# Kernel tuning notes

Hardware: AMD Instinct MI355X
Metric: run time of the kernel (lower is better)

## Reference

```python
import jax, jax.numpy as jnp
import numpy as np

B, C, H, W = 128, 3, 256, 256


def setup_inputs() -> dict:
    key = jax.random.key(0)
    k1, k2, k3, k4 = jax.random.split(key, 4)
    img = jax.random.uniform(k1, (B, C, H, W), jnp.float32)
    # init in the module: rot=PI, trans=0, scale=1, shear=0; add small noise
    rot = jnp.pi + 0.5 * jax.random.normal(k2, (B, 1), jnp.float32)
    trans = 0.1 * jax.random.normal(k3, (B, 2), jnp.float32)
    scale = jnp.ones((B, 1), jnp.float32)
    shear = 0.1 * jax.random.normal(k4, (B, 2), jnp.float32)
    return {"img": img, "rot": rot, "trans": trans, "scale": scale, "shear": shear}


def _theta(rot, trans, scale, shear):
    # 2x3 affine matrix per sample: A = scale * R(rot) @ Shear, last col = trans
    r = rot[:, 0]
    s = scale[:, 0]
    c, sn = jnp.cos(r), jnp.sin(r)
    shx, shy = shear[:, 0], shear[:, 1]
    a00 = s * (c - sn * shy)
    a01 = s * (c * shx - sn)
    a10 = s * (sn + c * shy)
    a11 = s * (sn * shx + c)
    row0 = jnp.stack([a00, a01, trans[:, 0]], axis=-1)  # [B,3]
    row1 = jnp.stack([a10, a11, trans[:, 1]], axis=-1)  # [B,3]
    return jnp.stack([row0, row1], axis=1)  # [B,2,3]


def _affine_grid(theta, Hc, Wc):
    # normalized coords, align_corners=False convention
    ys = (2.0 * (jnp.arange(Hc, dtype=jnp.float32) + 0.5) / Hc) - 1.0
    xs = (2.0 * (jnp.arange(Wc, dtype=jnp.float32) + 0.5) / Wc) - 1.0
    gx, gy = jnp.meshgrid(xs, ys)  # [H,W]
    base = jnp.stack([gx, gy, jnp.ones_like(gx)], axis=-1)  # [H,W,3]
    return jnp.einsum('bij,hwj->bhwi', theta, base)  # [B,H,W,2] -> (x,y)


def _grid_sample(img, grid):
    # bilinear, zeros padding, align_corners=False
    Bc, Cc, Hc, Wc = img.shape
    ix = ((grid[..., 0] + 1.0) * Wc - 1.0) / 2.0
    iy = ((grid[..., 1] + 1.0) * Hc - 1.0) / 2.0
    x0 = jnp.floor(ix); y0 = jnp.floor(iy)
    x1 = x0 + 1.0; y1 = y0 + 1.0
    wx1 = ix - x0; wx0 = 1.0 - wx1
    wy1 = iy - y0; wy0 = 1.0 - wy1
    flat = img.reshape(Bc, Cc, Hc * Wc)

    def gather(xi, yi, w):
        valid = (xi >= 0) & (xi <= Wc - 1) & (yi >= 0) & (yi <= Hc - 1)
        xc = jnp.clip(xi, 0, Wc - 1).astype(jnp.int32)
        yc = jnp.clip(yi, 0, Hc - 1).astype(jnp.int32)
        idx = (yc * Wc + xc).reshape(Bc, 1, -1)  # [B,1,H*W]
        vals = jnp.take_along_axis(flat, idx, axis=2)  # [B,C,H*W]
        wm = (w * valid.astype(w.dtype)).reshape(Bc, 1, -1)
        return vals * wm

    out = (gather(x0, y0, wx0 * wy0) + gather(x1, y0, wx1 * wy0)
           + gather(x0, y1, wx0 * wy1) + gather(x1, y1, wx1 * wy1))
    return out.reshape(Bc, Cc, Hc, Wc)


def reference(img, rot, trans, scale, shear):
    theta = _theta(rot, trans, scale, shear)
    grid = _affine_grid(theta, img.shape[2], img.shape[3])
    return _grid_sample(img, grid)
```

## Files before the change

kernel.cpp:

```cpp
#include <hip/hip_runtime.h>
#include <math.h>

#define BATCH 128
#define CHAN  3
#define IMH   256
#define IMW   256
#define NXCD  8
#define TW    32
#define TH    16

#define BH_T   42
#define NC_MAX 44
#define ROWSTR 132

__global__ __launch_bounds__(256) void affine_sample_kernel(
        const float* __restrict__ img,
        const float* __restrict__ rot,
        const float* __restrict__ trans,
        const float* __restrict__ scale,
        const float* __restrict__ shear,
        float* __restrict__ out) {
    __shared__ float tile[BH_T * ROWSTR];

    const int NBLK = BATCH * 64;
    const int p = blockIdx.x;
    const int L = (p & (NXCD - 1)) * (NBLK / NXCD) + (p >> 3);

    const int b  = L >> 6;
    const int tl = L & 63;
    const int w0 = (tl & 7) * TW;
    const int h0 = (tl >> 3) * (2 * TH);

    const float r   = rot[b];
    const float s   = scale[b];
    const float shx = shear[2 * b + 0];
    const float shy = shear[2 * b + 1];
    const float txr = trans[2 * b + 0];
    const float tyr = trans[2 * b + 1];
    const float c  = __cosf(r);
    const float sn = __sinf(r);
    const float a00 = s * (c - sn * shy);
    const float a01 = s * (c * shx - sn);
    const float a10 = s * (sn + c * shy);
    const float a11 = s * (sn * shx + c);
    const float g0x = 1.0f / (float)IMW - 1.0f;
    const float g0y = 1.0f / (float)IMH - 1.0f;
    const float Cx = ((a00 * g0x + a01 * g0y + txr + 1.0f) * (float)IMW - 1.0f) * 0.5f;
    const float Cy = ((a10 * g0x + a11 * g0y + tyr + 1.0f) * (float)IMH - 1.0f) * 0.5f;
    const float hx = 15.5f * fabsf(a00) + 7.5f * fabsf(a01);
    const float hy = 15.5f * fabsf(a10) + 7.5f * fabsf(a11);

    const int t  = threadIdx.x;
    const int wq = w0 + (t & 31);
    const int hoff = (t >> 5) << 1;
    const int lx2 = (t & 31) << 1;
    const int lyr = t >> 5;
    const int plane = IMH * IMW;
    const float* ibase = img + (size_t)(b * CHAN) * plane;

    for (int half = 0; half < 2; ++half) {
        const int h0h = h0 + half * TH;

        const float ixc = Cx + a00 * ((float)w0 + 15.5f) + a01 * ((float)h0h + 7.5f);
        const float iyc = Cy + a10 * ((float)w0 + 15.5f) + a11 * ((float)h0h + 7.5f);
        const int xlu = (int)floorf(ixc - hx);
        const int xhu = (int)floorf(ixc + hx) + 1;
        const int ylu = (int)floorf(iyc - hy);
        const int yhu = (int)floorf(iyc + hy) + 1;
        const bool interior = (xlu >= 1) & (xhu <= IMW - 2) &
                              (ylu >= 1) & (yhu <= IMH - 2);

        const int x_lo = min(max(xlu, 0), IMW - 1);
        const int x_hi = min(max(xhu, 0), IMW - 1);
        const int y_lo = min(max(ylu, 0), IMH - 1);
        const int y_hi = min(max(yhu, 0), IMH - 1);
        const int xs  = (x_lo - 1) & ~1;
        const int ys  = y_lo - 1;
        const int ncs = x_hi + 2 - xs;
        const int nrs = y_hi + 2 - ys;
        const bool fits = (ncs <= NC_MAX) & (nrs <= BH_T);

        const int hq = h0h + hoff;
        const float ixa = Cx + a00 * (float)wq + a01 * (float)hq;
        const float iya = Cy + a10 * (float)wq + a11 * (float)hq;
        const float ixb = ixa + a01;
        const float iyb = iya + a11;

        const float x0fa = floorf(ixa), y0fa = floorf(iya);
        const float x0fb = floorf(ixb), y0fb = floorf(iyb);
        const float wx1a = ixa - x0fa, wy1a = iya - y0fa;
        const float wx1b = ixb - x0fb, wy1b = iyb - y0fb;
        const float wx0a = 1.0f - wx1a, wy0a = 1.0f - wy1a;
        const float wx0b = 1.0f - wx1b, wy0b = 1.0f - wy1b;

        float w00a, w10a, w01a, w11a, w00b, w10b, w01b, w11b;
        if (interior) {
            w00a = wx0a * wy0a; w10a = wx1a * wy0a;
            w01a = wx0a * wy1a; w11a = wx1a * wy1a;
            w00b = wx0b * wy0b; w10b = wx1b * wy0b;
            w01b = wx0b * wy1b; w11b = wx1b * wy1b;
        } else {
            const bool vx0a = (x0fa >= 0.0f) & (x0fa <= (float)(IMW - 1));
            const bool vx1a = (x0fa >= -1.0f) & (x0fa <= (float)(IMW - 2));
            const bool vy0a = (y0fa >= 0.0f) & (y0fa <= (float)(IMH - 1));
            const bool vy1a = (y0fa >= -1.0f) & (y0fa <= (float)(IMH - 2));
            w00a = (vx0a && vy0a) ? (wx0a * wy0a) : 0.0f;
            w10a = (vx1a && vy0a) ? (wx1a * wy0a) : 0.0f;
            w01a = (vx0a && vy1a) ? (wx0a * wy1a) : 0.0f;
            w11a = (vx1a && vy1a) ? (wx1a * wy1a) : 0.0f;
            const bool vx0b = (x0fb >= 0.0f) & (x0fb <= (float)(IMW - 1));
            const bool vx1b = (x0fb >= -1.0f) & (x0fb <= (float)(IMW - 2));
            const bool vy0b = (y0fb >= 0.0f) & (y0fb <= (float)(IMH - 1));
            const bool vy1b = (y0fb >= -1.0f) & (y0fb <= (float)(IMH - 2));
            w00b = (vx0b && vy0b) ? (wx0b * wy0b) : 0.0f;
            w10b = (vx1b && vy0b) ? (wx1b * wy0b) : 0.0f;
            w01b = (vx0b && vy1b) ? (wx0b * wy1b) : 0.0f;
            w11b = (vx1b && vy1b) ? (wx1b * wy1b) : 0.0f;
        }

        const int x0ia = (int)x0fa, y0ia = (int)y0fa;
        const int x0ib = (int)x0fb, y0ib = (int)y0fb;
        const int obase = (b * CHAN) * plane + hq * IMW + wq;

        if (half) __syncthreads();

        if (fits) {
            const int nrd = (nrs + 7) >> 3;
            const bool wcol = lx2 < ncs;
            const int xg = min(max(xs + lx2, 0), IMW - 2);
            for (int rr = 0; rr < nrd; ++rr) {
                const int dy = (rr << 3) + lyr;
                if (wcol & (dy < nrs)) {
                    const int yg = min(max(ys + dy, 0), IMH - 1);
                    const float* src = ibase + yg * IMW + xg;
                    const float2 v0 = *(const float2*)(src);
                    const float2 v1 = *(const float2*)(src + plane);
                    const float2 v2 = *(const float2*)(src + 2 * plane);
                    float* dst = &tile[dy * ROWSTR + lx2 * 3];
                    dst[0] = v0.x; dst[1] = v1.x; dst[2] = v2.x;
                    dst[3] = v0.y; dst[4] = v1.y; dst[5] = v2.y;
                }
            }
        }
        __syncthreads();

        if (fits) {
            int rxa, rya, rxb, ryb;
            if (interior) {
                rxa = x0ia - xs;  rya = y0ia - ys;
                rxb = x0ib - xs;  ryb = y0ib - ys;
            } else {
                rxa = min(max(x0ia - xs, 0), ncs - 2);
                rya = min(max(y0ia - ys, 0), nrs - 2);
                rxb = min(max(x0ib - xs, 0), ncs - 2);
                ryb = min(max(y0ib - ys, 0), nrs - 2);
            }
            const float* tpa = &tile[rya * ROWSTR + rxa * 3];
            const float* tpb = &tile[ryb * ROWSTR + rxb * 3];
#pragma unroll
            for (int cc = 0; cc < CHAN; ++cc) {
                const float va = w00a * tpa[cc]          + w10a * tpa[cc + 3]
                               + w01a * tpa[cc + ROWSTR] + w11a * tpa[cc + ROWSTR + 3];
                const float vb = w00b * tpb[cc]          + w10b * tpb[cc + 3]
                               + w01b * tpb[cc + ROWSTR] + w11b * tpb[cc + ROWSTR + 3];
                out[obase + cc * plane]       = va;
                out[obase + cc * plane + IMW] = vb;
            }
        } else {
            const int x0ca = min(max(x0ia, 0), IMW - 1);
            const int x1ca = min(max(x0ia + 1, 0), IMW - 1);
            const int y0ca = min(max(y0ia, 0), IMH - 1);
            const int y1ca = min(max(y0ia + 1, 0), IMH - 1);
            const int x0cb = min(max(x0ib, 0), IMW - 1);
            const int x1cb = min(max(x0ib + 1, 0), IMW - 1);
            const int y0cb = min(max(y0ib, 0), IMH - 1);
            const int y1cb = min(max(y0ib + 1, 0), IMH - 1);
#pragma unroll
            for (int cc = 0; cc < CHAN; ++cc) {
                const float* p2 = ibase + cc * plane;
                const float va = w00a * p2[y0ca * IMW + x0ca] + w10a * p2[y0ca * IMW + x1ca]
                               + w01a * p2[y1ca * IMW + x0ca] + w11a * p2[y1ca * IMW + x1ca];
                const float vb = w00b * p2[y0cb * IMW + x0cb] + w10b * p2[y0cb * IMW + x1cb]
                               + w01b * p2[y1cb * IMW + x0cb] + w11b * p2[y1cb * IMW + x1cb];
                out[obase + cc * plane]       = va;
                out[obase + cc * plane + IMW] = vb;
            }
        }
    }
}

extern "C" void kernel_launch(void* const* d_in, const int* in_sizes, int n_in,
                              void* d_out, int out_size, void* d_ws, size_t ws_size,
                              hipStream_t stream) {
    const float* img   = (const float*)d_in[0];
    const float* rot   = (const float*)d_in[1];
    const float* trans = (const float*)d_in[2];
    const float* scale = (const float*)d_in[3];
    const float* shear = (const float*)d_in[4];
    float* out = (float*)d_out;

    const int nblocks = BATCH * 64;
    affine_sample_kernel<<<nblocks, 256, 0, stream>>>(img, rot, trans, scale,
                                                      shear, out);
}
```

Measured before the change: 43.37 us.

## Split blocks to one tile each and software-pipeline the global-to-LDS staging loads

Each block used to process two 32x16 output tiles one after the other. It now handles a single tile, which doubles the grid to 16384 blocks and removes the per-half loop and one barrier. The tile staging loop also prefetches the next row group's float2 loads into registers before it writes the current group to shared memory, so global load latency overlaps with LDS stores. The cost is more blocks, each repeating the per-sample setup math, plus extra registers for the prefetched values.

```diff
diff --git a/kernel.cpp b/kernel.cpp
--- a/kernel.cpp
+++ b/kernel.cpp
@@ -22,14 +22,14 @@
         float* __restrict__ out) {
     __shared__ float tile[BH_T * ROWSTR];
 
-    const int NBLK = BATCH * 64;
+    const int NBLK = BATCH * (IMH / TH) * (IMW / TW);
     const int p = blockIdx.x;
     const int L = (p & (NXCD - 1)) * (NBLK / NXCD) + (p >> 3);
 
-    const int b  = L >> 6;
-    const int tl = L & 63;
+    const int b  = L >> 7;
+    const int tl = L & 127;
     const int w0 = (tl & 7) * TW;
-    const int h0 = (tl >> 3) * (2 * TH);
+    const int h0 = (tl >> 3) * TH;
 
     const float r   = rot[b];
     const float s   = scale[b];
@@ -50,141 +50,145 @@
     const float hx = 15.5f * fabsf(a00) + 7.5f * fabsf(a01);
     const float hy = 15.5f * fabsf(a10) + 7.5f * fabsf(a11);
 
+    const float ixc = Cx + a00 * ((float)w0 + 15.5f) + a01 * ((float)h0 + 7.5f);
+    const float iyc = Cy + a10 * ((float)w0 + 15.5f) + a11 * ((float)h0 + 7.5f);
+    const int xlu = (int)floorf(ixc - hx);
+    const int xhu = (int)floorf(ixc + hx) + 1;
+    const int ylu = (int)floorf(iyc - hy);
+    const int yhu = (int)floorf(iyc + hy) + 1;
+    const bool interior = (xlu >= 1) & (xhu <= IMW - 2) & (ylu >= 1) & (yhu <= IMH - 2);
+
+    const int x_lo = min(max(xlu, 0), IMW - 1);
+    const int x_hi = min(max(xhu, 0), IMW - 1);
+    const int y_lo = min(max(ylu, 0), IMH - 1);
+    const int y_hi = min(max(yhu, 0), IMH - 1);
+    const int xs  = (x_lo - 1) & ~1;
+    const int ys  = y_lo - 1;
+    const int ncs = x_hi + 2 - xs;
+    const int nrs = y_hi + 2 - ys;
+
     const int t  = threadIdx.x;
     const int wq = w0 + (t & 31);
-    const int hoff = (t >> 5) << 1;
-    const int lx2 = (t & 31) << 1;
-    const int lyr = t >> 5;
+    const int hq = h0 + ((t >> 5) << 1);
+    const float ixa = Cx + a00 * (float)wq + a01 * (float)hq;
+    const float iya = Cy + a10 * (float)wq + a11 * (float)hq;
+    const float ixb = ixa + a01;
+    const float iyb = iya + a11;
+
+    const float x0fa = floorf(ixa), y0fa = floorf(iya);
+    const float x0fb = floorf(ixb), y0fb = floorf(iyb);
+    const float wx1a = ixa - x0fa, wy1a = iya - y0fa;
+    const float wx1b = ixb - x0fb, wy1b = iyb - y0fb;
+    const float wx0a = 1.0f - wx1a, wy0a = 1.0f - wy1a;
+    const float wx0b = 1.0f - wx1b, wy0b = 1.0f - wy1b;
+
+    float w00a, w10a, w01a, w11a, w00b, w10b, w01b, w11b;
+    if (interior) {
+        w00a = wx0a * wy0a; w10a = wx1a * wy0a;
+        w01a = wx0a * wy1a; w11a = wx1a * wy1a;
+        w00b = wx0b * wy0b; w10b = wx1b * wy0b;
+        w01b = wx0b * wy1b; w11b = wx1b * wy1b;
+    } else {
+        const bool vx0a = (x0fa >= 0.0f) & (x0fa <= (float)(IMW - 1));
+        const bool vx1a = (x0fa >= -1.0f) & (x0fa <= (float)(IMW - 2));
+        const bool vy0a = (y0fa >= 0.0f) & (y0fa <= (float)(IMH - 1));
+        const bool vy1a = (y0fa >= -1.0f) & (y0fa <= (float)(IMH - 2));
+        w00a = (vx0a && vy0a) ? (wx0a * wy0a) : 0.0f;
+        w10a = (vx1a && vy0a) ? (wx1a * wy0a) : 0.0f;
+        w01a = (vx0a && vy1a) ? (wx0a * wy1a) : 0.0f;
+        w11a = (vx1a && vy1a) ? (wx1a * wy1a) : 0.0f;
+        const bool vx0b = (x0fb >= 0.0f) & (x0fb <= (float)(IMW - 1));
+        const bool vx1b = (x0fb >= -1.0f) & (x0fb <= (float)(IMW - 2));
+        const bool vy0b = (y0fb >= 0.0f) & (y0fb <= (float)(IMH - 1));
+        const bool vy1b = (y0fb >= -1.0f) & (y0fb <= (float)(IMH - 2));
+        w00b = (vx0b && vy0b) ? (wx0b * wy0b) : 0.0f;
+        w10b = (vx1b && vy0b) ? (wx1b * wy0b) : 0.0f;
+        w01b = (vx0b && vy1b) ? (wx0b * wy1b) : 0.0f;
+        w11b = (vx1b && vy1b) ? (wx1b * wy1b) : 0.0f;
+    }
+
+    const int x0ia = (int)x0fa, y0ia = (int)y0fa;
+    const int x0ib = (int)x0fb, y0ib = (int)y0fb;
+
     const int plane = IMH * IMW;
+    const int obase = (b * CHAN) * plane + hq * IMW + wq;
     const float* ibase = img + (size_t)(b * CHAN) * plane;
 
-    for (int half = 0; half < 2; ++half) {
-        const int h0h = h0 + half * TH;
-
-        const float ixc = Cx + a00 * ((float)w0 + 15.5f) + a01 * ((float)h0h + 7.5f);
-        const float iyc = Cy + a10 * ((float)w0 + 15.5f) + a11 * ((float)h0h + 7.5f);
-        const int xlu = (int)floorf(ixc - hx);
-        const int xhu = (int)floorf(ixc + hx) + 1;
-        const int ylu = (int)floorf(iyc - hy);
-        const int yhu = (int)floorf(iyc + hy) + 1;
-        const bool interior = (xlu >= 1) & (xhu <= IMW - 2) &
-                              (ylu >= 1) & (yhu <= IMH - 2);
-
-        const int x_lo = min(max(xlu, 0), IMW - 1);
-        const int x_hi = min(max(xhu, 0), IMW - 1);
-        const int y_lo = min(max(ylu, 0), IMH - 1);
-        const int y_hi = min(max(yhu, 0), IMH - 1);
-        const int xs  = (x_lo - 1) & ~1;
-        const int ys  = y_lo - 1;
-        const int ncs = x_hi + 2 - xs;
-        const int nrs = y_hi + 2 - ys;
-        const bool fits = (ncs <= NC_MAX) & (nrs <= BH_T);
-
-        const int hq = h0h + hoff;
-        const float ixa = Cx + a00 * (float)wq + a01 * (float)hq;
-        const float iya = Cy + a10 * (float)wq + a11 * (float)hq;
-        const float ixb = ixa + a01;
-        const float iyb = iya + a11;
-
-        const float x0fa = floorf(ixa), y0fa = floorf(iya);
-        const float x0fb = floorf(ixb), y0fb = floorf(iyb);
-        const float wx1a = ixa - x0fa, wy1a = iya - y0fa;
-        const float wx1b = ixb - x0fb, wy1b = iyb - y0fb;
-        const float wx0a = 1.0f - wx1a, wy0a = 1.0f - wy1a;
-        const float wx0b = 1.0f - wx1b, wy0b = 1.0f - wy1b;
-
-        float w00a, w10a, w01a, w11a, w00b, w10b, w01b, w11b;
+    if (ncs <= NC_MAX && nrs <= BH_T) {
+        const int lx2 = (t & 31) << 1;
+        const int lyr = t >> 5;
+        const int nrd = (nrs + 7) >> 3;
+        const bool wcol = lx2 < ncs;
+        const int xg = min(max(xs + lx2, 0), IMW - 2);
+
+        float2 v0, v1, v2;
+        {
+            const int dy = lyr;
+            const int yg = min(max(ys + dy, 0), IMH - 1);
+            const float* src = ibase + yg * IMW + xg;
+            if (wcol) { v0 = *(const float2*)(src);
+                        v1 = *(const float2*)(src + plane);
+                        v2 = *(const float2*)(src + 2 * plane); }
+        }
+        for (int rr = 0; rr < nrd; ++rr) {
+            const int dy = (rr << 3) + lyr;
+            float2 n0, n1, n2;
+            const int dyn = dy + 8;
+            if ((rr + 1 < nrd) & wcol & (dyn < nrs)) {
+                const int yg = min(max(ys + dyn, 0), IMH - 1);
+                const float* src = ibase + yg * IMW + xg;
+                n0 = *(const float2*)(src);
+                n1 = *(const float2*)(src + plane);
+                n2 = *(const float2*)(src + 2 * plane);
+            }
+            if (wcol & (dy < nrs)) {
+                float* dst = &tile[dy * ROWSTR + lx2 * 3];
+                dst[0] = v0.x; dst[1] = v1.x; dst[2] = v2.x;
+                dst[3] = v0.y; dst[4] = v1.y; dst[5] = v2.y;
+            }
+            v0 = n0; v1 = n1; v2 = n2;
+        }
+        __syncthreads();
+
+        int rxa, rya, rxb, ryb;
         if (interior) {
-            w00a = wx0a * wy0a; w10a = wx1a * wy0a;
-            w01a = wx0a * wy1a; w11a = wx1a * wy1a;
-            w00b = wx0b * wy0b; w10b = wx1b * wy0b;
-            w01b = wx0b * wy1b; w11b = wx1b * wy1b;
+            rxa = x0ia - xs;  rya = y0ia - ys;
+            rxb = x0ib - xs;  ryb = y0ib - ys;
         } else {
-            const bool vx0a = (x0fa >= 0.0f) & (x0fa <= (float)(IMW - 1));
-            const bool vx1a = (x0fa >= -1.0f) & (x0fa <= (float)(IMW - 2));
-            const bool vy0a = (y0fa >= 0.0f) & (y0fa <= (float)(IMH - 1));
-            const bool vy1a = (y0fa >= -1.0f) & (y0fa <= (float)(IMH - 2));
-            w00a = (vx0a && vy0a) ? (wx0a * wy0a) : 0.0f;
-            w10a = (vx1a && vy0a) ? (wx1a * wy0a) : 0.0f;
-            w01a = (vx0a && vy1a) ? (wx0a * wy1a) : 0.0f;
-            w11a = (vx1a && vy1a) ? (wx1a * wy1a) : 0.0f;
-            const bool vx0b = (x0fb >= 0.0f) & (x0fb <= (float)(IMW - 1));
-            const bool vx1b = (x0fb >= -1.0f) & (x0fb <= (float)(IMW - 2));
-            const bool vy0b = (y0fb >= 0.0f) & (y0fb <= (float)(IMH - 1));
-            const bool vy1b = (y0fb >= -1.0f) & (y0fb <= (float)(IMH - 2));
-            w00b = (vx0b && vy0b) ? (wx0b * wy0b) : 0.0f;
-            w10b = (vx1b && vy0b) ? (wx1b * wy0b) : 0.0f;
-            w01b = (vx0b && vy1b) ? (wx0b * wy1b) : 0.0f;
-            w11b = (vx1b && vy1b) ? (wx1b * wy1b) : 0.0f;
-        }
-
-        const int x0ia = (int)x0fa, y0ia = (int)y0fa;
-        const int x0ib = (int)x0fb, y0ib = (int)y0fb;
-        const int obase = (b * CHAN) * plane + hq * IMW + wq;
-
-        if (half) __syncthreads();
-
-        if (fits) {
-            const int nrd = (nrs + 7) >> 3;
-            const bool wcol = lx2 < ncs;
-            const int xg = min(max(xs + lx2, 0), IMW - 2);
-            for (int rr = 0; rr < nrd; ++rr) {
-                const int dy = (rr << 3) + lyr;
-                if (wcol & (dy < nrs)) {
-                    const int yg = min(max(ys + dy, 0), IMH - 1);
-                    const float* src = ibase + yg * IMW + xg;
-                    const float2 v0 = *(const float2*)(src);
-                    const float2 v1 = *(const float2*)(src + plane);
-                    const float2 v2 = *(const float2*)(src + 2 * plane);
-                    float* dst = &tile[dy * ROWSTR + lx2 * 3];
-                    dst[0] = v0.x; dst[1] = v1.x; dst[2] = v2.x;
-                    dst[3] = v0.y; dst[4] = v1.y; dst[5] = v2.y;
-                }
-            }
-        }
-        __syncthreads();
-
-        if (fits) {
-            int rxa, rya, rxb, ryb;
-            if (interior) {
-                rxa = x0ia - xs;  rya = y0ia - ys;
-                rxb = x0ib - xs;  ryb = y0ib - ys;
-            } else {
-                rxa = min(max(x0ia - xs, 0), ncs - 2);
-                rya = min(max(y0ia - ys, 0), nrs - 2);
-                rxb = min(max(x0ib - xs, 0), ncs - 2);
-                ryb = min(max(y0ib - ys, 0), nrs - 2);
-            }
-            const float* tpa = &tile[rya * ROWSTR + rxa * 3];
-            const float* tpb = &tile[ryb * ROWSTR + rxb * 3];
+            rxa = min(max(x0ia - xs, 0), ncs - 2);
+            rya = min(max(y0ia - ys, 0), nrs - 2);
+            rxb = min(max(x0ib - xs, 0), ncs - 2);
+            ryb = min(max(y0ib - ys, 0), nrs - 2);
+        }
+        const float* tpa = &tile[rya * ROWSTR + rxa * 3];
+        const float* tpb = &tile[ryb * ROWSTR + rxb * 3];
 #pragma unroll
-            for (int cc = 0; cc < CHAN; ++cc) {
-                const float va = w00a * tpa[cc]          + w10a * tpa[cc + 3]
-                               + w01a * tpa[cc + ROWSTR] + w11a * tpa[cc + ROWSTR + 3];
-                const float vb = w00b * tpb[cc]          + w10b * tpb[cc + 3]
-                               + w01b * tpb[cc + ROWSTR] + w11b * tpb[cc + ROWSTR + 3];
-                out[obase + cc * plane]       = va;
-                out[obase + cc * plane + IMW] = vb;
-            }
-        } else {
-            const int x0ca = min(max(x0ia, 0), IMW - 1);
-            const int x1ca = min(max(x0ia + 1, 0), IMW - 1);
-            const int y0ca = min(max(y0ia, 0), IMH - 1);
-            const int y1ca = min(max(y0ia + 1, 0), IMH - 1);
-            const int x0cb = min(max(x0ib, 0), IMW - 1);
-            const int x1cb = min(max(x0ib + 1, 0), IMW - 1);
-            const int y0cb = min(max(y0ib, 0), IMH - 1);
-            const int y1cb = min(max(y0ib + 1, 0), IMH - 1);
+        for (int cc = 0; cc < CHAN; ++cc) {
+            const float va = w00a * tpa[cc]          + w10a * tpa[cc + 3]
+                           + w01a * tpa[cc + ROWSTR] + w11a * tpa[cc + ROWSTR + 3];
+            const float vb = w00b * tpb[cc]          + w10b * tpb[cc + 3]
+                           + w01b * tpb[cc + ROWSTR] + w11b * tpb[cc + ROWSTR + 3];
+            out[obase + cc * plane]       = va;
+            out[obase + cc * plane + IMW] = vb;
+        }
+    } else {
+        const int x0ca = min(max(x0ia, 0), IMW - 1);
+        const int x1ca = min(max(x0ia + 1, 0), IMW - 1);
+        const int y0ca = min(max(y0ia, 0), IMH - 1);
+        const int y1ca = min(max(y0ia + 1, 0), IMH - 1);
+        const int x0cb = min(max(x0ib, 0), IMW - 1);
+        const int x1cb = min(max(x0ib + 1, 0), IMW - 1);
+        const int y0cb = min(max(y0ib, 0), IMH - 1);
+        const int y1cb = min(max(y0ib + 1, 0), IMH - 1);
 #pragma unroll
-            for (int cc = 0; cc < CHAN; ++cc) {
-                const float* p2 = ibase + cc * plane;
-                const float va = w00a * p2[y0ca * IMW + x0ca] + w10a * p2[y0ca * IMW + x1ca]
-                               + w01a * p2[y1ca * IMW + x0ca] + w11a * p2[y1ca * IMW + x1ca];
-                const float vb = w00b * p2[y0cb * IMW + x0cb] + w10b * p2[y0cb * IMW + x1cb]
-                               + w01b * p2[y1cb * IMW + x0cb] + w11b * p2[y1cb * IMW + x1cb];
-                out[obase + cc * plane]       = va;
-                out[obase + cc * plane + IMW] = vb;
-            }
+        for (int cc = 0; cc < CHAN; ++cc) {
+            const float* p2 = ibase + cc * plane;
+            const float va = w00a * p2[y0ca * IMW + x0ca] + w10a * p2[y0ca * IMW + x1ca]
+                           + w01a * p2[y1ca * IMW + x0ca] + w11a * p2[y1ca * IMW + x1ca];
+            const float vb = w00b * p2[y0cb * IMW + x0cb] + w10b * p2[y0cb * IMW + x1cb]
+                           + w01b * p2[y1cb * IMW + x0cb] + w11b * p2[y1cb * IMW + x1cb];
+            out[obase + cc * plane]       = va;
+            out[obase + cc * plane + IMW] = vb;
         }
     }
 }
@@ -199,7 +203,7 @@
     const float* shear = (const float*)d_in[4];
     float* out = (float*)d_out;
 
-    const int nblocks = BATCH * 64;
+    const int nblocks = BATCH * (IMH / TH) * (IMW / TW);
     affine_sample_kernel<<<nblocks, 256, 0, stream>>>(img, rot, trans, scale,
                                                       shear, out);
 }
```

After: 41.44 us. -4.4%, faster.

## Switch to persistent blocks looping over tiles with XCD-aware partitioning and packed float2 math

Applied to the files above, without the earlier changes.

Replaces the one-block-per-tile grid with 1792 persistent blocks. Each block walks a contiguous run of 9 or 10 tiles of 32x16 pixels, and tiles are partitioned per XCD so neighbouring tiles share an L2. Per-batch affine parameters are recomputed only when the batch index changes. The bilinear weights and the tile interpolation are packed into float2 operations to encourage packed FP32 math, and interior tiles skip the clamping in the staging loop. This trades launch and occupancy flexibility for lower per-block setup cost, but it may load-balance worse and serialise the load-then-compute phases within a block.

```diff
diff --git a/kernel.cpp b/kernel.cpp
--- a/kernel.cpp
+++ b/kernel.cpp
@@ -12,6 +12,12 @@
 #define BH_T   42
 #define NC_MAX 44
 #define ROWSTR 132
+
+#define PBLK   1792
+#define BPX    224
+#define TPX    2048
+#define QT     9
+#define RT     32
 
 __global__ __launch_bounds__(256) void affine_sample_kernel(
         const float* __restrict__ img,
@@ -22,47 +28,56 @@
         float* __restrict__ out) {
     __shared__ float tile[BH_T * ROWSTR];
 
-    const int NBLK = BATCH * 64;
-    const int p = blockIdx.x;
-    const int L = (p & (NXCD - 1)) * (NBLK / NXCD) + (p >> 3);
-
-    const int b  = L >> 6;
-    const int tl = L & 63;
-    const int w0 = (tl & 7) * TW;
-    const int h0 = (tl >> 3) * (2 * TH);
-
-    const float r   = rot[b];
-    const float s   = scale[b];
-    const float shx = shear[2 * b + 0];
-    const float shy = shear[2 * b + 1];
-    const float txr = trans[2 * b + 0];
-    const float tyr = trans[2 * b + 1];
-    const float c  = __cosf(r);
-    const float sn = __sinf(r);
-    const float a00 = s * (c - sn * shy);
-    const float a01 = s * (c * shx - sn);
-    const float a10 = s * (sn + c * shy);
-    const float a11 = s * (sn * shx + c);
-    const float g0x = 1.0f / (float)IMW - 1.0f;
-    const float g0y = 1.0f / (float)IMH - 1.0f;
-    const float Cx = ((a00 * g0x + a01 * g0y + txr + 1.0f) * (float)IMW - 1.0f) * 0.5f;
-    const float Cy = ((a10 * g0x + a11 * g0y + tyr + 1.0f) * (float)IMH - 1.0f) * 0.5f;
-    const float hx = 15.5f * fabsf(a00) + 7.5f * fabsf(a01);
-    const float hy = 15.5f * fabsf(a10) + 7.5f * fabsf(a11);
-
-    const int t  = threadIdx.x;
-    const int wq = w0 + (t & 31);
+    const int pxcd = blockIdx.x & (NXCD - 1);
+    const int j    = blockIdx.x >> 3;
+    const int cnt  = (j < RT) ? (QT + 1) : QT;
+    const int off  = (j < RT) ? j * (QT + 1) : RT * (QT + 1) + (j - RT) * QT;
+    const int Lbase = pxcd * TPX + off;
+
+    const int t    = threadIdx.x;
+    const int wl   = t & 31;
     const int hoff = (t >> 5) << 1;
-    const int lx2 = (t & 31) << 1;
-    const int lyr = t >> 5;
+    const int lx2  = wl << 1;
+    const int lyr  = t >> 5;
     const int plane = IMH * IMW;
-    const float* ibase = img + (size_t)(b * CHAN) * plane;
-
-    for (int half = 0; half < 2; ++half) {
-        const int h0h = h0 + half * TH;
-
-        const float ixc = Cx + a00 * ((float)w0 + 15.5f) + a01 * ((float)h0h + 7.5f);
-        const float iyc = Cy + a10 * ((float)w0 + 15.5f) + a11 * ((float)h0h + 7.5f);
+
+    int bcur = -1;
+    float a00 = 0.f, a01 = 0.f, a10 = 0.f, a11 = 0.f;
+    float Cx = 0.f, Cy = 0.f, hx = 0.f, hy = 0.f;
+    const float* ibase = img;
+
+    for (int k = 0; k < cnt; ++k) {
+        const int L  = Lbase + k;
+        const int b  = L >> 7;
+        const int tl = L & 127;
+        const int w0 = (tl & 7) * TW;
+        const int h0 = (tl >> 3) * TH;
+
+        if (b != bcur) {
+            bcur = b;
+            const float r   = rot[b];
+            const float s   = scale[b];
+            const float shx = shear[2 * b + 0];
+            const float shy = shear[2 * b + 1];
+            const float txr = trans[2 * b + 0];
+            const float tyr = trans[2 * b + 1];
+            const float c  = __cosf(r);
+            const float sn = __sinf(r);
+            a00 = s * (c - sn * shy);
+            a01 = s * (c * shx - sn);
+            a10 = s * (sn + c * shy);
+            a11 = s * (sn * shx + c);
+            const float g0x = 1.0f / (float)IMW - 1.0f;
+            const float g0y = 1.0f / (float)IMH - 1.0f;
+            Cx = ((a00 * g0x + a01 * g0y + txr + 1.0f) * (float)IMW - 1.0f) * 0.5f;
+            Cy = ((a10 * g0x + a11 * g0y + tyr + 1.0f) * (float)IMH - 1.0f) * 0.5f;
+            hx = 15.5f * fabsf(a00) + 7.5f * fabsf(a01);
+            hy = 15.5f * fabsf(a10) + 7.5f * fabsf(a11);
+            ibase = img + (size_t)(b * CHAN) * plane;
+        }
+
+        const float ixc = Cx + a00 * ((float)w0 + 15.5f) + a01 * ((float)h0 + 7.5f);
+        const float iyc = Cy + a10 * ((float)w0 + 15.5f) + a11 * ((float)h0 + 7.5f);
         const int xlu = (int)floorf(ixc - hx);
         const int xhu = (int)floorf(ixc + hx) + 1;
         const int ylu = (int)floorf(iyc - hy);
@@ -80,65 +95,78 @@
         const int nrs = y_hi + 2 - ys;
         const bool fits = (ncs <= NC_MAX) & (nrs <= BH_T);
 
-        const int hq = h0h + hoff;
+        const int wq = w0 + wl;
+        const int hq = h0 + hoff;
         const float ixa = Cx + a00 * (float)wq + a01 * (float)hq;
         const float iya = Cy + a10 * (float)wq + a11 * (float)hq;
-        const float ixb = ixa + a01;
-        const float iyb = iya + a11;
-
-        const float x0fa = floorf(ixa), y0fa = floorf(iya);
-        const float x0fb = floorf(ixb), y0fb = floorf(iyb);
-        const float wx1a = ixa - x0fa, wy1a = iya - y0fa;
-        const float wx1b = ixb - x0fb, wy1b = iyb - y0fb;
-        const float wx0a = 1.0f - wx1a, wy0a = 1.0f - wy1a;
-        const float wx0b = 1.0f - wx1b, wy0b = 1.0f - wy1b;
-
-        float w00a, w10a, w01a, w11a, w00b, w10b, w01b, w11b;
-        if (interior) {
-            w00a = wx0a * wy0a; w10a = wx1a * wy0a;
-            w01a = wx0a * wy1a; w11a = wx1a * wy1a;
-            w00b = wx0b * wy0b; w10b = wx1b * wy0b;
-            w01b = wx0b * wy1b; w11b = wx1b * wy1b;
-        } else {
-            const bool vx0a = (x0fa >= 0.0f) & (x0fa <= (float)(IMW - 1));
-            const bool vx1a = (x0fa >= -1.0f) & (x0fa <= (float)(IMW - 2));
-            const bool vy0a = (y0fa >= 0.0f) & (y0fa <= (float)(IMH - 1));
-            const bool vy1a = (y0fa >= -1.0f) & (y0fa <= (float)(IMH - 2));
-            w00a = (vx0a && vy0a) ? (wx0a * wy0a) : 0.0f;
-            w10a = (vx1a && vy0a) ? (wx1a * wy0a) : 0.0f;
-            w01a = (vx0a && vy1a) ? (wx0a * wy1a) : 0.0f;
-            w11a = (vx1a && vy1a) ? (wx1a * wy1a) : 0.0f;
-            const bool vx0b = (x0fb >= 0.0f) & (x0fb <= (float)(IMW - 1));
-            const bool vx1b = (x0fb >= -1.0f) & (x0fb <= (float)(IMW - 2));
-            const bool vy0b = (y0fb >= 0.0f) & (y0fb <= (float)(IMH - 1));
-            const bool vy1b = (y0fb >= -1.0f) & (y0fb <= (float)(IMH - 2));
-            w00b = (vx0b && vy0b) ? (wx0b * wy0b) : 0.0f;
-            w10b = (vx1b && vy0b) ? (wx1b * wy0b) : 0.0f;
-            w01b = (vx0b && vy1b) ? (wx0b * wy1b) : 0.0f;
-            w11b = (vx1b && vy1b) ? (wx1b * wy1b) : 0.0f;
-        }
-
-        const int x0ia = (int)x0fa, y0ia = (int)y0fa;
-        const int x0ib = (int)x0fb, y0ib = (int)y0fb;
+        const float2 ixv = {ixa, ixa + a01};
+        const float2 iyv = {iya, iya + a11};
+        const float2 x0fv = {floorf(ixv.x), floorf(ixv.y)};
+        const float2 y0fv = {floorf(iyv.x), floorf(iyv.y)};
+        const float2 wx1v = ixv - x0fv;
+        const float2 wy1v = iyv - y0fv;
+        const float2 onev = {1.0f, 1.0f};
+        const float2 wx0v = onev - wx1v;
+        const float2 wy0v = onev - wy1v;
+        float2 w00v = wx0v * wy0v;
+        float2 w10v = wx1v * wy0v;
+        float2 w01v = wx0v * wy1v;
+        float2 w11v = wx1v * wy1v;
+        if (!interior) {
+            const bool vx0a = (x0fv.x >= 0.0f) & (x0fv.x <= (float)(IMW - 1));
+            const bool vx1a = (x0fv.x >= -1.0f) & (x0fv.x <= (float)(IMW - 2));
+            const bool vy0a = (y0fv.x >= 0.0f) & (y0fv.x <= (float)(IMH - 1));
+            const bool vy1a = (y0fv.x >= -1.0f) & (y0fv.x <= (float)(IMH - 2));
+            if (!(vx0a && vy0a)) w00v.x = 0.0f;
+            if (!(vx1a && vy0a)) w10v.x = 0.0f;
+            if (!(vx0a && vy1a)) w01v.x = 0.0f;
+            if (!(vx1a && vy1a)) w11v.x = 0.0f;
+            const bool vx0b = (x0fv.y >= 0.0f) & (x0fv.y <= (float)(IMW - 1));
+            const bool vx1b = (x0fv.y >= -1.0f) & (x0fv.y <= (float)(IMW - 2));
+            const bool vy0b = (y0fv.y >= 0.0f) & (y0fv.y <= (float)(IMH - 1));
+            const bool vy1b = (y0fv.y >= -1.0f) & (y0fv.y <= (float)(IMH - 2));
+            if (!(vx0b && vy0b)) w00v.y = 0.0f;
+            if (!(vx1b && vy0b)) w10v.y = 0.0f;
+            if (!(vx0b && vy1b)) w01v.y = 0.0f;
+            if (!(vx1b && vy1b)) w11v.y = 0.0f;
+        }
+        const int x0ia = (int)x0fv.x, y0ia = (int)y0fv.x;
+        const int x0ib = (int)x0fv.y, y0ib = (int)y0fv.y;
         const int obase = (b * CHAN) * plane + hq * IMW + wq;
 
-        if (half) __syncthreads();
+        if (k) __syncthreads();
 
         if (fits) {
             const int nrd = (nrs + 7) >> 3;
             const bool wcol = lx2 < ncs;
-            const int xg = min(max(xs + lx2, 0), IMW - 2);
-            for (int rr = 0; rr < nrd; ++rr) {
-                const int dy = (rr << 3) + lyr;
-                if (wcol & (dy < nrs)) {
-                    const int yg = min(max(ys + dy, 0), IMH - 1);
-                    const float* src = ibase + yg * IMW + xg;
-                    const float2 v0 = *(const float2*)(src);
-                    const float2 v1 = *(const float2*)(src + plane);
-                    const float2 v2 = *(const float2*)(src + 2 * plane);
-                    float* dst = &tile[dy * ROWSTR + lx2 * 3];
-                    dst[0] = v0.x; dst[1] = v1.x; dst[2] = v2.x;
-                    dst[3] = v0.y; dst[4] = v1.y; dst[5] = v2.y;
+            if (interior) {
+                const float* colp = ibase + (xs + lx2);
+                for (int rr = 0; rr < nrd; ++rr) {
+                    const int dy = (rr << 3) + lyr;
+                    if (wcol & (dy < nrs)) {
+                        const float* src = colp + (ys + dy) * IMW;
+                        const float2 v0 = *(const float2*)(src);
+                        const float2 v1 = *(const float2*)(src + plane);
+                        const float2 v2 = *(const float2*)(src + 2 * plane);
+                        float* dst = &tile[dy * ROWSTR + lx2 * 3];
+                        dst[0] = v0.x; dst[1] = v1.x; dst[2] = v2.x;
+                        dst[3] = v0.y; dst[4] = v1.y; dst[5] = v2.y;
+                    }
+                }
+            } else {
+                const int xg = min(max(xs + lx2, 0), IMW - 2);
+                for (int rr = 0; rr < nrd; ++rr) {
+                    const int dy = (rr << 3) + lyr;
+                    if (wcol & (dy < nrs)) {
+                        const int yg = min(max(ys + dy, 0), IMH - 1);
+                        const float* src = ibase + yg * IMW + xg;
+                        const float2 v0 = *(const float2*)(src);
+                        const float2 v1 = *(const float2*)(src + plane);
+                        const float2 v2 = *(const float2*)(src + 2 * plane);
+                        float* dst = &tile[dy * ROWSTR + lx2 * 3];
+                        dst[0] = v0.x; dst[1] = v1.x; dst[2] = v2.x;
+                        dst[3] = v0.y; dst[4] = v1.y; dst[5] = v2.y;
+                    }
                 }
             }
         }
@@ -159,12 +187,14 @@
             const float* tpb = &tile[ryb * ROWSTR + rxb * 3];
 #pragma unroll
             for (int cc = 0; cc < CHAN; ++cc) {
-                const float va = w00a * tpa[cc]          + w10a * tpa[cc + 3]
-                               + w01a * tpa[cc + ROWSTR] + w11a * tpa[cc + ROWSTR + 3];
-                const float vb = w00b * tpb[cc]          + w10b * tpb[cc + 3]
-                               + w01b * tpb[cc + ROWSTR] + w11b * tpb[cc + ROWSTR + 3];
-                out[obase + cc * plane]       = va;
-                out[obase + cc * plane + IMW] = vb;
+                const float2 t00 = {tpa[cc],          tpb[cc]};
+                const float2 t10 = {tpa[cc + 3],      tpb[cc + 3]};
+                const float2 t01 = {tpa[cc + ROWSTR], tpb[cc + ROWSTR]};
+                const float2 t11 = {tpa[cc + ROWSTR + 3], tpb[cc + ROWSTR + 3]};
+                const float2 v = w00v * t00 + w10v * t10
+                               + w01v * t01 + w11v * t11;
+                out[obase + cc * plane]       = v.x;
+                out[obase + cc * plane + IMW] = v.y;
             }
         } else {
             const int x0ca = min(max(x0ia, 0), IMW - 1);
@@ -178,10 +208,10 @@
 #pragma unroll
             for (int cc = 0; cc < CHAN; ++cc) {
                 const float* p2 = ibase + cc * plane;
-                const float va = w00a * p2[y0ca * IMW + x0ca] + w10a * p2[y0ca * IMW + x1ca]
-                               + w01a * p2[y1ca * IMW + x0ca] + w11a * p2[y1ca * IMW + x1ca];
-                const float vb = w00b * p2[y0cb * IMW + x0cb] + w10b * p2[y0cb * IMW + x1cb]
-                               + w01b * p2[y1cb * IMW + x0cb] + w11b * p2[y1cb * IMW + x1cb];
+                const float va = w00v.x * p2[y0ca * IMW + x0ca] + w10v.x * p2[y0ca * IMW + x1ca]
+                               + w01v.x * p2[y1ca * IMW + x0ca] + w11v.x * p2[y1ca * IMW + x1ca];
+                const float vb = w00v.y * p2[y0cb * IMW + x0cb] + w10v.y * p2[y0cb * IMW + x1cb]
+                               + w01v.y * p2[y1cb * IMW + x0cb] + w11v.y * p2[y1cb * IMW + x1cb];
                 out[obase + cc * plane]       = va;
                 out[obase + cc * plane + IMW] = vb;
             }
@@ -199,7 +229,6 @@
     const float* shear = (const float*)d_in[4];
     float* out = (float*)d_out;
 
-    const int nblocks = BATCH * 64;
-    affine_sample_kernel<<<nblocks, 256, 0, stream>>>(img, rot, trans, scale,
-                                                      shear, out);
+    affine_sample_kernel<<<PBLK, 256, 0, stream>>>(img, rot, trans, scale,
+                                                   shear, out);
 }
```

New measurement: 51.92 us. 1.2x slower.
